# Kernel optimization log

Measured on AMD Instinct MI355X. Metric: run time of the kernel, lower is better.

The kernel has to match this reference:

```python
import jax, jax.numpy as jnp
import numpy as np

TEMP1, TEMP2, TEMP3 = 4.0, 5.0, 10.0  # forward() default temps
EPS = 1e-8


def setup_inputs() -> dict:
    key = jax.random.key(0)
    k1, k2 = jax.random.split(key)
    B, L, D = 64, 64, 512
    return {
        "ecg_embs": jax.random.normal(k1, (B, L, D), dtype=jnp.float32),
        "sent_embs": jax.random.normal(k2, (B, L, D), dtype=jnp.float32),
    }


def reference(ecg_embs, sent_embs):
    # Fully-batched version of the original per-sample Python loop.
    # i indexes the sentence (query) sample, j the ecg (context) sample.
    B, L, D = ecg_embs.shape
    # scores[i,j,s,q] = <ecg[j,s,:], sent[i,q,:]>  == contextT @ query in torch
    scores = jnp.einsum('jsd,iqd->ijsq', ecg_embs, sent_embs)
    # 1st softmax over query axis q
    attn = jax.nn.softmax(scores, axis=-1)
    # transpose to (i,j,q,s), temperature-scale, 2nd softmax over source axis s
    attn = jax.nn.softmax(TEMP1 * jnp.swapaxes(attn, -1, -2), axis=-1)  # (i,j,q,s)
    # weightedContext[i,j,q,:] = sum_s attn[i,j,q,s] * ecg[j,s,:]
    wctx = jnp.einsum('ijqs,jsd->ijqd', attn, ecg_embs)
    sent = sent_embs[:, None]  # (i,1,q,d) broadcast over j
    w12 = jnp.sum(sent * wctx, axis=-1)
    w1 = jnp.linalg.norm(sent, axis=-1)
    w2 = jnp.linalg.norm(wctx, axis=-1)
    cos = w12 / jnp.maximum(w1 * w2, EPS)  # (i,j,q)
    # row_sim.mul_(temp2).exp_().sum(dim=1).log() ; similarities[j,i] (cat along dim=1)
    sim = TEMP3 * jnp.log(jnp.sum(jnp.exp(TEMP2 * cos), axis=-1)).T  # (j,i)
    labels = jnp.arange(B)
    logp0 = jax.nn.log_softmax(sim, axis=-1)
    logp1 = jax.nn.log_softmax(sim.T, axis=-1)
    loss0 = -jnp.mean(logp0[labels, labels])
    loss1 = -jnp.mean(logp1[labels, labels])
    # att_maps: list of attn[i] from iteration i == diagonal (i==j) attention,
    # each shaped (1, queryL, ih=1, iw=sourceL); stacked -> (B, 1, L, 1, L)
    att_maps = attn[labels, labels][:, None, :, None, :]
    return (loss0 + loss1) / 2.0, att_maps
```

## Files before the change

### kernel.cpp

```cpp
#include <hip/hip_runtime.h>
#include <math.h>

typedef __attribute__((ext_vector_type(8))) short short8;
typedef __attribute__((ext_vector_type(4))) float f32x4;
typedef unsigned int uint;
typedef unsigned short ushort;

#define T1 4.0f
#define T2 5.0f
#define T3 10.0f
#define EPSF 1e-8f
#define SST 68

__device__ inline ushort f2bf(float x) {
    union { float f; uint u; } a; a.f = x;
    uint r = a.u + 0x7FFFu + ((a.u >> 16) & 1u);
    return (ushort)(r >> 16);
}
__device__ inline float bf2f(ushort h) {
    union { uint u; float f; } a; a.u = ((uint)h) << 16;
    return a.f;
}

#define GLDS(gsrc, ldst) \
    __builtin_amdgcn_global_load_lds( \
        (const __attribute__((address_space(1))) uint*)(gsrc), \
        (__attribute__((address_space(3))) uint*)(ldst), 16, 0, 0)

__global__ __launch_bounds__(256) void prep_kernel(
        const float* __restrict__ ecg, const float* __restrict__ sent,
        char* __restrict__ EH, char* __restrict__ EL,
        char* __restrict__ SH, char* __restrict__ SL, float* __restrict__ w1) {
    __shared__ float partial[256];
    const int bid = blockIdx.x;
    const int tensor = bid >> 6, idx = bid & 63;
    const float* src = (tensor ? sent : ecg) + (size_t)idx * 32768;
    char* dh = (tensor ? SH : EH) + (size_t)idx * 65536;
    char* dl = (tensor ? SL : EL) + (size_t)idx * 65536;
    const int tid = threadIdx.x;
    const int r = tid & 63;
    float s2 = 0.f;
    #pragma unroll
    for (int it = 0; it < 4; it++) {
        int kc = it * 4 + (tid >> 6);
        const float* p = src + r * 512 + kc * 32;
        char* oh = dh + kc * 4096 + r * 64;
        char* ol = dl + kc * 4096 + r * 64;
        #pragma unroll
        for (int c = 0; c < 4; c++) {
            float4 v0 = *(const float4*)(p + c * 8);
            float4 v1 = *(const float4*)(p + c * 8 + 4);
            float x[8] = {v0.x, v0.y, v0.z, v0.w, v1.x, v1.y, v1.z, v1.w};
            uint hw[4], lw[4];
            #pragma unroll
            for (int e = 0; e < 4; e++) {
                float a0 = x[2 * e], a1 = x[2 * e + 1];
                ushort h0 = f2bf(a0), h1 = f2bf(a1);
                hw[e] = (uint)h0 | ((uint)h1 << 16);
                ushort l0 = f2bf(a0 - bf2f(h0)), l1 = f2bf(a1 - bf2f(h1));
                lw[e] = (uint)l0 | ((uint)l1 << 16);
                s2 += a0 * a0 + a1 * a1;
            }
            int phys = (c + (r >> 1)) & 3;
            uint4 H; H.x = hw[0]; H.y = hw[1]; H.z = hw[2]; H.w = hw[3];
            *(uint4*)(oh + phys * 16) = H;
            uint4 L; L.x = lw[0]; L.y = lw[1]; L.z = lw[2]; L.w = lw[3];
            *(uint4*)(ol + phys * 16) = L;
        }
    }
    partial[tid] = s2;
    __syncthreads();
    if (tensor == 1 && tid < 64) {
        float t = partial[tid] + partial[tid + 64] + partial[tid + 128] + partial[tid + 192];
        w1[idx * 64 + tid] = sqrtf(t);
    }
}

__global__ __launch_bounds__(256) void gprep_kernel(
        const char* __restrict__ EH, const char* __restrict__ EL, char* __restrict__ Gp) {
    __shared__ __align__(16) char lds[8192];
    const int j = blockIdx.x;
    const int tid = threadIdx.x;
    const int wv = tid >> 6, lane = tid & 63;
    const int wq = wv >> 1, wn = wv & 1;
    const int quad = lane >> 4, ln = lane & 15;
    const char* srcH = EH + (size_t)j * 65536 + wv * 1024 + lane * 16;
    const char* srcL = EL + (size_t)j * 65536 + wv * 1024 + lane * 16;

    int ao[2], bo[2];
    #pragma unroll
    for (int mi = 0; mi < 2; mi++) {
        int R = 32 * wq + 16 * mi + ln;
        ao[mi] = R * 64 + ((quad + (R >> 1)) & 3) * 16;
    }
    #pragma unroll
    for (int ni = 0; ni < 2; ni++) {
        int R = 32 * wn + 16 * ni + ln;
        bo[ni] = R * 64 + ((quad + (R >> 1)) & 3) * 16;
    }

    f32x4 acc[2][2];
    #pragma unroll
    for (int a = 0; a < 2; a++)
        #pragma unroll
        for (int b = 0; b < 2; b++) acc[a][b] = (f32x4){0.f, 0.f, 0.f, 0.f};

    for (int kc = 0; kc < 16; kc++) {
        GLDS(srcH + (size_t)kc * 4096, lds + wv * 1024);
        GLDS(srcL + (size_t)kc * 4096, lds + 4096 + wv * 1024);
        __syncthreads();
        short8 ah[2], al[2], bh[2], bl[2];
        #pragma unroll
        for (int mi = 0; mi < 2; mi++) {
            ah[mi] = *(const short8*)(lds + ao[mi]);
            al[mi] = *(const short8*)(lds + 4096 + ao[mi]);
        }
        #pragma unroll
        for (int ni = 0; ni < 2; ni++) {
            bh[ni] = *(const short8*)(lds + bo[ni]);
            bl[ni] = *(const short8*)(lds + 4096 + bo[ni]);
        }
        #pragma unroll
        for (int mi = 0; mi < 2; mi++)
            #pragma unroll
            for (int ni = 0; ni < 2; ni++) {
                acc[mi][ni] = __builtin_amdgcn_mfma_f32_16x16x32_bf16(ah[mi], bh[ni], acc[mi][ni], 0, 0, 0);
                acc[mi][ni] = __builtin_amdgcn_mfma_f32_16x16x32_bf16(ah[mi], bl[ni], acc[mi][ni], 0, 0, 0);
                acc[mi][ni] = __builtin_amdgcn_mfma_f32_16x16x32_bf16(al[mi], bh[ni], acc[mi][ni], 0, 0, 0);
            }
        __syncthreads();
    }
    #pragma unroll
    for (int mi = 0; mi < 2; mi++)
        #pragma unroll
        for (int ni = 0; ni < 2; ni++)
            #pragma unroll
            for (int r = 0; r < 4; r++) {
                int t = 32 * wq + 16 * mi + quad * 4 + r;
                int u = 32 * wn + 16 * ni + ln;
                float g = acc[mi][ni][r];
                ushort h = f2bf(g);
                ushort l = f2bf(g - bf2f(h));
                char* base = Gp + (size_t)j * 16384 + t * 128 + (((u >> 3) + t) & 7) * 16 + (u & 7) * 2;
                *(ushort*)base = h;
                *(ushort*)(base + 8192) = l;
            }
}

__global__ __launch_bounds__(256, 4) void pair_kernel(
        const char* __restrict__ EH, const char* __restrict__ EL,
        const char* __restrict__ SH, const char* __restrict__ SL,
        const char* __restrict__ Gp, const float* __restrict__ w1g,
        float* __restrict__ simval, float* __restrict__ out) {

    __shared__ __align__(16) char lds[33792];
    __shared__ __align__(16) float mz[64];
    __shared__ float w12all[256], w2all[256];

    const int tid = threadIdx.x;
    const int bn = blockIdx.x;
    const int xcd = bn & 7, slot = bn >> 3;
    const int T = xcd * 8 + (slot >> 4);
    const int wp = slot & 15;
    const int bi = (T >> 3) * 4 + (wp >> 2);
    const int bj = (T & 7) * 4 + (wp & 3);
    const int i0 = bi * 2, j0 = bj * 2;

    const int wv = tid >> 6, lane = tid & 63;
    const int wq = wv >> 1, wn = wv & 1;
    const int quad = lane >> 4, ln = lane & 15;

    int aoff[4], boff[4];
    #pragma unroll
    for (int mi = 0; mi < 4; mi++) {
        int R = 64 * (mi >> 1) + 32 * wq + 16 * (mi & 1) + ln;
        aoff[mi] = R * 64 + ((quad + (R >> 1)) & 3) * 16;
    }
    #pragma unroll
    for (int ni = 0; ni < 4; ni++) {
        int R = 64 * (ni >> 1) + 32 * wn + 16 * (ni & 1) + ln;
        boff[ni] = 16384 + R * 64 + ((quad + (R >> 1)) & 3) * 16;
    }

    const char* gA; const char* gB; int ldoff;
    if (wv == 0)      { gA = EH + (size_t)j0 * 65536;       gB = EH + (size_t)(j0 + 1) * 65536; ldoff = 0; }
    else if (wv == 1) { gA = EL + (size_t)j0 * 65536;       gB = EL + (size_t)(j0 + 1) * 65536; ldoff = 8192; }
    else if (wv == 2) { gA = SH + (size_t)i0 * 65536;       gB = SH + (size_t)(i0 + 1) * 65536; ldoff = 16384; }
    else              { gA = SL + (size_t)i0 * 65536;       gB = SL + (size_t)(i0 + 1) * 65536; ldoff = 24576; }
    gA += lane * 16; gB += lane * 16;

    f32x4 acc[4][4];
    #pragma unroll
    for (int a = 0; a < 4; a++)
        #pragma unroll
        for (int b = 0; b < 4; b++) acc[a][b] = (f32x4){0.f, 0.f, 0.f, 0.f};

    for (int kc = 0; kc < 16; kc++) {
        #pragma unroll
        for (int n = 0; n < 4; n++) GLDS(gA + n * 1024, lds + ldoff + n * 1024);
        #pragma unroll
        for (int n = 0; n < 4; n++) GLDS(gB + n * 1024, lds + ldoff + 4096 + n * 1024);
        gA += 4096; gB += 4096;
        __syncthreads();
        short8 bh[4], bl[4];
        #pragma unroll
        for (int ni = 0; ni < 4; ni++) {
            bh[ni] = *(const short8*)(lds + boff[ni]);
            bl[ni] = *(const short8*)(lds + boff[ni] + 8192);
        }
        #pragma unroll
        for (int mi = 0; mi < 4; mi++) {
            short8 ah = *(const short8*)(lds + aoff[mi]);
            short8 al = *(const short8*)(lds + aoff[mi] + 8192);
            #pragma unroll
            for (int ni = 0; ni < 4; ni++) {
                acc[mi][ni] = __builtin_amdgcn_mfma_f32_16x16x32_bf16(ah, bh[ni], acc[mi][ni], 0, 0, 0);
                acc[mi][ni] = __builtin_amdgcn_mfma_f32_16x16x32_bf16(ah, bl[ni], acc[mi][ni], 0, 0, 0);
                acc[mi][ni] = __builtin_amdgcn_mfma_f32_16x16x32_bf16(al, bh[ni], acc[mi][ni], 0, 0, 0);
            }
        }
        __syncthreads();
    }

    float* SsT = (float*)lds;
    float* yT  = (float*)lds;
    char*  Pb  = lds + 17408;

    #pragma unroll
    for (int pr = 0; pr < 4; pr++) {
        const int a = pr >> 1, b = pr & 1;
        const int i = i0 + b, j = j0 + a;

        #pragma unroll
        for (int dm = 0; dm < 2; dm++)
            #pragma unroll
            for (int dn = 0; dn < 2; dn++) {
                int s0 = 32 * wq + 16 * dm + quad * 4;
                int q  = 32 * wn + 16 * dn + ln;
                *(f32x4*)(SsT + q * SST + s0) = acc[2 * a + dm][2 * b + dn];
            }
        __syncthreads();

        {
            const int s = tid >> 2, c = tid & 3;
            float vv[16]; float m = -1e30f;
            #pragma unroll
            for (int t = 0; t < 16; t++) { vv[t] = SsT[(16 * c + t) * SST + s]; m = fmaxf(m, vv[t]); }
            m = fmaxf(m, __shfl_xor(m, 1));
            m = fmaxf(m, __shfl_xor(m, 2));
            float sum = 0.f;
            #pragma unroll
            for (int t = 0; t < 16; t++) sum += __expf(vv[t] - m);
            sum += __shfl_xor(sum, 1);
            sum += __shfl_xor(sum, 2);
            if (c == 0) mz[s] = m + __logf(sum);
        }
        __syncthreads();

        {
            const int q = tid >> 2, c = tid & 3;
            float sc[16], at[16];
            #pragma unroll
            for (int r4 = 0; r4 < 4; r4++)
                *(f32x4*)(sc + 4 * r4) = *(const f32x4*)(SsT + q * SST + 16 * c + 4 * r4);
            float mzv[16];
            #pragma unroll
            for (int r4 = 0; r4 < 4; r4++)
                *(f32x4*)(mzv + 4 * r4) = *(const f32x4*)(mz + 16 * c + 4 * r4);
            float m2 = -1e30f;
            #pragma unroll
            for (int t = 0; t < 16; t++) {
                at[t] = __expf(sc[t] - mzv[t]);
                m2 = fmaxf(m2, T1 * at[t]);
            }
            m2 = fmaxf(m2, __shfl_xor(m2, 1));
            m2 = fmaxf(m2, __shfl_xor(m2, 2));
            float sum = 0.f;
            #pragma unroll
            for (int t = 0; t < 16; t++) { at[t] = __expf(T1 * at[t] - m2); sum += at[t]; }
            sum += __shfl_xor(sum, 1);
            sum += __shfl_xor(sum, 2);
            float inv = 1.f / sum;
            float p12 = 0.f;
            #pragma unroll
            for (int t = 0; t < 16; t++) { at[t] *= inv; p12 += at[t] * sc[t]; }
            p12 += __shfl_xor(p12, 1);
            p12 += __shfl_xor(p12, 2);
            if (c == 0) w12all[pr * 64 + q] = p12;

            if (i == j) {
                float* om = out + 1 + (size_t)i * 4096;
                #pragma unroll
                for (int t = 0; t < 16; t++) om[q * 64 + c * 16 + t] = at[t];
            }

            uint hw[8], lw[8];
            #pragma unroll
            for (int e = 0; e < 8; e++) {
                ushort h0 = f2bf(at[2 * e]), h1 = f2bf(at[2 * e + 1]);
                hw[e] = (uint)h0 | ((uint)h1 << 16);
                ushort l0 = f2bf(at[2 * e] - bf2f(h0)), l1 = f2bf(at[2 * e + 1] - bf2f(h1));
                lw[e] = (uint)l0 | ((uint)l1 << 16);
            }
            int p0 = (2 * c + q) & 7, p1 = (2 * c + 1 + q) & 7;
            uint4 W;
            W.x = hw[0]; W.y = hw[1]; W.z = hw[2]; W.w = hw[3];
            *(uint4*)(Pb + q * 128 + p0 * 16) = W;
            W.x = hw[4]; W.y = hw[5]; W.z = hw[6]; W.w = hw[7];
            *(uint4*)(Pb + q * 128 + p1 * 16) = W;
            W.x = lw[0]; W.y = lw[1]; W.z = lw[2]; W.w = lw[3];
            *(uint4*)(Pb + 8192 + q * 128 + p0 * 16) = W;
            W.x = lw[4]; W.y = lw[5]; W.z = lw[6]; W.w = lw[7];
            *(uint4*)(Pb + 8192 + q * 128 + p1 * 16) = W;
        }
        __syncthreads();

        {
            const char* gs = Gp + (size_t)j * 16384 + tid * 64;
            char* gd = lds + tid * 64;
            uint4 g0 = *(const uint4*)(gs);
            uint4 g1 = *(const uint4*)(gs + 16);
            uint4 g2 = *(const uint4*)(gs + 32);
            uint4 g3 = *(const uint4*)(gs + 48);
            *(uint4*)(gd)      = g0;
            *(uint4*)(gd + 16) = g1;
            *(uint4*)(gd + 32) = g2;
            *(uint4*)(gd + 48) = g3;
        }
        __syncthreads();

        f32x4 acc2[2][2];
        #pragma unroll
        for (int x = 0; x < 2; x++)
            #pragma unroll
            for (int y = 0; y < 2; y++) acc2[x][y] = (f32x4){0.f, 0.f, 0.f, 0.f};
        #pragma unroll
        for (int ch = 0; ch < 2; ch++) {
            short8 pah[2], pal[2], gbh[2], gbl[2];
            #pragma unroll
            for (int m2i = 0; m2i < 2; m2i++) {
                int q = 32 * wq + 16 * m2i + ln;
                int ph = ((ch * 4 + quad) + q) & 7;
                pah[m2i] = *(const short8*)(Pb + q * 128 + ph * 16);
                pal[m2i] = *(const short8*)(Pb + 8192 + q * 128 + ph * 16);
            }
            #pragma unroll
            for (int n2i = 0; n2i < 2; n2i++) {
                int u = 32 * wn + 16 * n2i + ln;
                int ph = ((ch * 4 + quad) + u) & 7;
                gbh[n2i] = *(const short8*)(lds + u * 128 + ph * 16);
                gbl[n2i] = *(const short8*)(lds + 8192 + u * 128 + ph * 16);
            }
            #pragma unroll
            for (int m2i = 0; m2i < 2; m2i++)
                #pragma unroll
                for (int n2i = 0; n2i < 2; n2i++) {
                    acc2[m2i][n2i] = __builtin_amdgcn_mfma_f32_16x16x32_bf16(pah[m2i], gbh[n2i], acc2[m2i][n2i], 0, 0, 0);
                    acc2[m2i][n2i] = __builtin_amdgcn_mfma_f32_16x16x32_bf16(pah[m2i], gbl[n2i], acc2[m2i][n2i], 0, 0, 0);
                    acc2[m2i][n2i] = __builtin_amdgcn_mfma_f32_16x16x32_bf16(pal[m2i], gbh[n2i], acc2[m2i][n2i], 0, 0, 0);
                }
        }
        __syncthreads();

        #pragma unroll
        for (int m2i = 0; m2i < 2; m2i++)
            #pragma unroll
            for (int n2i = 0; n2i < 2; n2i++) {
                int q0 = 32 * wq + 16 * m2i + quad * 4;
                int t  = 32 * wn + 16 * n2i + ln;
                *(f32x4*)(yT + t * SST + q0) = acc2[m2i][n2i];
            }
        __syncthreads();

        {
            const int q = tid >> 2, c = tid & 3;
            int p0 = (2 * c + q) & 7, p1 = (2 * c + 1 + q) & 7;
            uint4 H0 = *(const uint4*)(Pb + q * 128 + p0 * 16);
            uint4 H1 = *(const uint4*)(Pb + q * 128 + p1 * 16);
            uint4 L0 = *(const uint4*)(Pb + 8192 + q * 128 + p0 * 16);
            uint4 L1 = *(const uint4*)(Pb + 8192 + q * 128 + p1 * 16);
            uint hw[8] = {H0.x,H0.y,H0.z,H0.w, H1.x,H1.y,H1.z,H1.w};
            uint lw[8] = {L0.x,L0.y,L0.z,L0.w, L1.x,L1.y,L1.z,L1.w};
            float s = 0.f;
            #pragma unroll
            for (int e = 0; e < 8; e++) {
                float q0v = bf2f((ushort)(hw[e] & 0xFFFFu)) + bf2f((ushort)(lw[e] & 0xFFFFu));
                float q1v = bf2f((ushort)(hw[e] >> 16))     + bf2f((ushort)(lw[e] >> 16));
                s += q0v * yT[(16 * c + 2 * e) * SST + q];
                s += q1v * yT[(16 * c + 2 * e + 1) * SST + q];
            }
            s += __shfl_xor(s, 1);
            s += __shfl_xor(s, 2);
            if (c == 0) w2all[pr * 64 + q] = s;
        }
        __syncthreads();
    }

    {
        const int pr = wv;
        const int ii = i0 + (pr & 1), jj = j0 + (pr >> 1);
        float w2 = sqrtf(fmaxf(w2all[pr * 64 + lane], 0.f));
        float cosv = w12all[pr * 64 + lane] / fmaxf(w1g[ii * 64 + lane] * w2, EPSF);
        float e = __expf(T2 * cosv);
        #pragma unroll
        for (int off = 32; off; off >>= 1) e += __shfl_down(e, off);
        if (lane == 0) simval[ii * 64 + jj] = T3 * __logf(e);
    }
}

__global__ __launch_bounds__(256) void loss_kernel(const float* __restrict__ val,
                                                   float* __restrict__ out) {
    __shared__ float v[4096];
    const int tid = threadIdx.x;
    #pragma unroll
    for (int k = 0; k < 4; k++)
        ((float4*)v)[tid + k * 256] = ((const float4*)val)[tid + k * 256];
    __syncthreads();
    if (tid < 64) {
        int i = tid;
        float rmax = -1e30f, cmax = -1e30f;
        for (int jj = 0; jj < 64; jj++) {
            rmax = fmaxf(rmax, v[i * 64 + jj]);
            cmax = fmaxf(cmax, v[jj * 64 + i]);
        }
        float rs = 0.f, cs = 0.f;
        for (int jj = 0; jj < 64; jj++) {
            rs += __expf(v[i * 64 + jj] - rmax);
            cs += __expf(v[jj * 64 + i] - cmax);
        }
        float rlse = rmax + __logf(rs);
        float clse = cmax + __logf(cs);
        float part = 2.f * v[i * 64 + i] - rlse - clse;
        #pragma unroll
        for (int off = 32; off; off >>= 1) part += __shfl_down(part, off);
        if (i == 0) out[0] = -part / 128.f;
    }
}

extern "C" void kernel_launch(void* const* d_in, const int* in_sizes, int n_in,
                              void* d_out, int out_size, void* d_ws, size_t ws_size,
                              hipStream_t stream) {
    (void)in_sizes; (void)n_in; (void)out_size; (void)ws_size;
    const float* ecg  = (const float*)d_in[0];
    const float* sent = (const float*)d_in[1];
    float* out = (float*)d_out;

    char* ws = (char*)d_ws;
    float* w1v  = (float*)ws;
    float* simv = (float*)(ws + 16384);
    char* EH = ws + 32768;
    char* EL = EH + (size_t)64 * 65536;
    char* SH = EL + (size_t)64 * 65536;
    char* SL = SH + (size_t)64 * 65536;
    char* Gp = SL + (size_t)64 * 65536;

    prep_kernel <<<128, 256, 0, stream>>>(ecg, sent, EH, EL, SH, SL, w1v);
    gprep_kernel<<<64,  256, 0, stream>>>(EH, EL, Gp);
    pair_kernel <<<1024, 256, 0, stream>>>(EH, EL, SH, SL, Gp, w1v, simv, out);
    loss_kernel <<<1,   256, 0, stream>>>(simv, out);
}
```

Before: 152.3 us.

## Switch pair kernel to 32x32 MFMA tiles and fold G prep into prep kernel

Both matrix products in the pair kernel now use 32x32x16 bf16 MFMA with 16-wide accumulators instead of 16x16x32 tiles, and the LDS fragment offsets are rewritten to match. The aim is fewer LDS fragment reads and MFMA issues per output. The separate gprep kernel is merged into the ecg half of prep_kernel, which saves a launch. That fused path now reads EH/EL straight from global memory that the same block has just written, and its correctness depends on global writes being visible within the block after the barrier. Two smaller changes: the Gp tile loads are issued early, before the softmax, to hide their latency, and the softmax column reads are staggered per thread group to reduce LDS bank conflicts.

Measured after the change: 156.7 us. +2.9%, slower.

```diff
diff --git a/kernel.cpp b/kernel.cpp
--- a/kernel.cpp
+++ b/kernel.cpp
@@ -3,6 +3,7 @@
 
 typedef __attribute__((ext_vector_type(8))) short short8;
 typedef __attribute__((ext_vector_type(4))) float f32x4;
+typedef __attribute__((ext_vector_type(16))) float f32x16;
 typedef unsigned int uint;
 typedef unsigned short ushort;
 
@@ -30,7 +31,8 @@
 __global__ __launch_bounds__(256) void prep_kernel(
         const float* __restrict__ ecg, const float* __restrict__ sent,
         char* __restrict__ EH, char* __restrict__ EL,
-        char* __restrict__ SH, char* __restrict__ SL, float* __restrict__ w1) {
+        char* __restrict__ SH, char* __restrict__ SL,
+        char* __restrict__ Gp, float* __restrict__ w1) {
     __shared__ float partial[256];
     const int bid = blockIdx.x;
     const int tensor = bid >> 6, idx = bid & 63;
@@ -70,81 +72,79 @@
     }
     partial[tid] = s2;
     __syncthreads();
-    if (tensor == 1 && tid < 64) {
-        float t = partial[tid] + partial[tid + 64] + partial[tid + 128] + partial[tid + 192];
-        w1[idx * 64 + tid] = sqrtf(t);
-    }
-}
-
-__global__ __launch_bounds__(256) void gprep_kernel(
-        const char* __restrict__ EH, const char* __restrict__ EL, char* __restrict__ Gp) {
-    __shared__ __align__(16) char lds[8192];
-    const int j = blockIdx.x;
-    const int tid = threadIdx.x;
-    const int wv = tid >> 6, lane = tid & 63;
-    const int wq = wv >> 1, wn = wv & 1;
-    const int quad = lane >> 4, ln = lane & 15;
-    const char* srcH = EH + (size_t)j * 65536 + wv * 1024 + lane * 16;
-    const char* srcL = EL + (size_t)j * 65536 + wv * 1024 + lane * 16;
-
-    int ao[2], bo[2];
-    #pragma unroll
-    for (int mi = 0; mi < 2; mi++) {
-        int R = 32 * wq + 16 * mi + ln;
-        ao[mi] = R * 64 + ((quad + (R >> 1)) & 3) * 16;
-    }
-    #pragma unroll
-    for (int ni = 0; ni < 2; ni++) {
-        int R = 32 * wn + 16 * ni + ln;
-        bo[ni] = R * 64 + ((quad + (R >> 1)) & 3) * 16;
-    }
-
-    f32x4 acc[2][2];
-    #pragma unroll
-    for (int a = 0; a < 2; a++)
-        #pragma unroll
-        for (int b = 0; b < 2; b++) acc[a][b] = (f32x4){0.f, 0.f, 0.f, 0.f};
-
-    for (int kc = 0; kc < 16; kc++) {
-        GLDS(srcH + (size_t)kc * 4096, lds + wv * 1024);
-        GLDS(srcL + (size_t)kc * 4096, lds + 4096 + wv * 1024);
-        __syncthreads();
-        short8 ah[2], al[2], bh[2], bl[2];
+    if (tensor == 1) {
+        if (tid < 64) {
+            float t = partial[tid] + partial[tid + 64] + partial[tid + 128] + partial[tid + 192];
+            w1[idx * 64 + tid] = sqrtf(t);
+        }
+        return;
+    }
+
+    {
+        const char* srcH = EH + (size_t)idx * 65536;
+        const char* srcL = EL + (size_t)idx * 65536;
+        const int wv = tid >> 6, lane = tid & 63;
+        const int wq = wv >> 1, wn = wv & 1;
+        const int quad = lane >> 4, ln = lane & 15;
+
+        int ao[2], bo[2];
         #pragma unroll
         for (int mi = 0; mi < 2; mi++) {
-            ah[mi] = *(const short8*)(lds + ao[mi]);
-            al[mi] = *(const short8*)(lds + 4096 + ao[mi]);
+            int R = 32 * wq + 16 * mi + ln;
+            ao[mi] = R * 64 + ((quad + (R >> 1)) & 3) * 16;
         }
         #pragma unroll
         for (int ni = 0; ni < 2; ni++) {
-            bh[ni] = *(const short8*)(lds + bo[ni]);
-            bl[ni] = *(const short8*)(lds + 4096 + bo[ni]);
+            int R = 32 * wn + 16 * ni + ln;
+            bo[ni] = R * 64 + ((quad + (R >> 1)) & 3) * 16;
+        }
+
+        f32x4 acc[2][2];
+        #pragma unroll
+        for (int a = 0; a < 2; a++)
+            #pragma unroll
+            for (int b = 0; b < 2; b++) acc[a][b] = (f32x4){0.f, 0.f, 0.f, 0.f};
+
+        #pragma unroll 2
+        for (int kc = 0; kc < 16; kc++) {
+            const char* ph = srcH + (size_t)kc * 4096;
+            const char* pl = srcL + (size_t)kc * 4096;
+            short8 ah[2], al[2], bh[2], bl[2];
+            #pragma unroll
+            for (int mi = 0; mi < 2; mi++) {
+                ah[mi] = *(const short8*)(ph + ao[mi]);
+                al[mi] = *(const short8*)(pl + ao[mi]);
+            }
+            #pragma unroll
+            for (int ni = 0; ni < 2; ni++) {
+                bh[ni] = *(const short8*)(ph + bo[ni]);
+                bl[ni] = *(const short8*)(pl + bo[ni]);
+            }
+            #pragma unroll
+            for (int mi = 0; mi < 2; mi++)
+                #pragma unroll
+                for (int ni = 0; ni < 2; ni++) {
+                    acc[mi][ni] = __builtin_amdgcn_mfma_f32_16x16x32_bf16(ah[mi], bh[ni], acc[mi][ni], 0, 0, 0);
+                    acc[mi][ni] = __builtin_amdgcn_mfma_f32_16x16x32_bf16(ah[mi], bl[ni], acc[mi][ni], 0, 0, 0);
+                    acc[mi][ni] = __builtin_amdgcn_mfma_f32_16x16x32_bf16(al[mi], bh[ni], acc[mi][ni], 0, 0, 0);
+                }
         }
         #pragma unroll
         for (int mi = 0; mi < 2; mi++)
             #pragma unroll
-            for (int ni = 0; ni < 2; ni++) {
-                acc[mi][ni] = __builtin_amdgcn_mfma_f32_16x16x32_bf16(ah[mi], bh[ni], acc[mi][ni], 0, 0, 0);
-                acc[mi][ni] = __builtin_amdgcn_mfma_f32_16x16x32_bf16(ah[mi], bl[ni], acc[mi][ni], 0, 0, 0);
-                acc[mi][ni] = __builtin_amdgcn_mfma_f32_16x16x32_bf16(al[mi], bh[ni], acc[mi][ni], 0, 0, 0);
-            }
-        __syncthreads();
-    }
-    #pragma unroll
-    for (int mi = 0; mi < 2; mi++)
-        #pragma unroll
-        for (int ni = 0; ni < 2; ni++)
-            #pragma unroll
-            for (int r = 0; r < 4; r++) {
-                int t = 32 * wq + 16 * mi + quad * 4 + r;
-                int u = 32 * wn + 16 * ni + ln;
-                float g = acc[mi][ni][r];
-                ushort h = f2bf(g);
-                ushort l = f2bf(g - bf2f(h));
-                char* base = Gp + (size_t)j * 16384 + t * 128 + (((u >> 3) + t) & 7) * 16 + (u & 7) * 2;
-                *(ushort*)base = h;
-                *(ushort*)(base + 8192) = l;
-            }
+            for (int ni = 0; ni < 2; ni++)
+                #pragma unroll
+                for (int rr = 0; rr < 4; rr++) {
+                    int t = 32 * wq + 16 * mi + quad * 4 + rr;
+                    int u = 32 * wn + 16 * ni + ln;
+                    float g = acc[mi][ni][rr];
+                    ushort h = f2bf(g);
+                    ushort l = f2bf(g - bf2f(h));
+                    char* base = Gp + (size_t)idx * 16384 + t * 128 + (((u >> 3) + t) & 7) * 16 + (u & 7) * 2;
+                    *(ushort*)base = h;
+                    *(ushort*)(base + 8192) = l;
+                }
+    }
 }
 
 __global__ __launch_bounds__(256, 4) void pair_kernel(
@@ -168,19 +168,19 @@
 
     const int wv = tid >> 6, lane = tid & 63;
     const int wq = wv >> 1, wn = wv & 1;
-    const int quad = lane >> 4, ln = lane & 15;
-
-    int aoff[4], boff[4];
+    const int l5 = lane >> 5, l31 = lane & 31;
+
+    int aoff[2][2], boff[2][2];
     #pragma unroll
-    for (int mi = 0; mi < 4; mi++) {
-        int R = 64 * (mi >> 1) + 32 * wq + 16 * (mi & 1) + ln;
-        aoff[mi] = R * 64 + ((quad + (R >> 1)) & 3) * 16;
-    }
-    #pragma unroll
-    for (int ni = 0; ni < 4; ni++) {
-        int R = 64 * (ni >> 1) + 32 * wn + 16 * (ni & 1) + ln;
-        boff[ni] = 16384 + R * 64 + ((quad + (R >> 1)) & 3) * 16;
-    }
+    for (int ti = 0; ti < 2; ti++)
+        #pragma unroll
+        for (int kh = 0; kh < 2; kh++) {
+            int cc = l5 + 2 * kh;
+            int Ra = 64 * ti + 32 * wq + l31;
+            aoff[ti][kh] = Ra * 64 + ((cc + (Ra >> 1)) & 3) * 16;
+            int Rb = 64 * ti + 32 * wn + l31;
+            boff[ti][kh] = 16384 + Rb * 64 + ((cc + (Rb >> 1)) & 3) * 16;
+        }
 
     const char* gA; const char* gB; int ldoff;
     if (wv == 0)      { gA = EH + (size_t)j0 * 65536;       gB = EH + (size_t)(j0 + 1) * 65536; ldoff = 0; }
@@ -189,11 +189,9 @@
     else              { gA = SL + (size_t)i0 * 65536;       gB = SL + (size_t)(i0 + 1) * 65536; ldoff = 24576; }
     gA += lane * 16; gB += lane * 16;
 
-    f32x4 acc[4][4];
-    #pragma unroll
-    for (int a = 0; a < 4; a++)
-        #pragma unroll
-        for (int b = 0; b < 4; b++) acc[a][b] = (f32x4){0.f, 0.f, 0.f, 0.f};
+    const f32x16 zf = {0.f,0.f,0.f,0.f,0.f,0.f,0.f,0.f,0.f,0.f,0.f,0.f,0.f,0.f,0.f,0.f};
+    f32x16 acc[2][2];
+    acc[0][0] = zf; acc[0][1] = zf; acc[1][0] = zf; acc[1][1] = zf;
 
     for (int kc = 0; kc < 16; kc++) {
         #pragma unroll
@@ -202,22 +200,30 @@
         for (int n = 0; n < 4; n++) GLDS(gB + n * 1024, lds + ldoff + 4096 + n * 1024);
         gA += 4096; gB += 4096;
         __syncthreads();
-        short8 bh[4], bl[4];
-        #pragma unroll
-        for (int ni = 0; ni < 4; ni++) {
-            bh[ni] = *(const short8*)(lds + boff[ni]);
-            bl[ni] = *(const short8*)(lds + boff[ni] + 8192);
-        }
-        #pragma unroll
-        for (int mi = 0; mi < 4; mi++) {
-            short8 ah = *(const short8*)(lds + aoff[mi]);
-            short8 al = *(const short8*)(lds + aoff[mi] + 8192);
-            #pragma unroll
-            for (int ni = 0; ni < 4; ni++) {
-                acc[mi][ni] = __builtin_amdgcn_mfma_f32_16x16x32_bf16(ah, bh[ni], acc[mi][ni], 0, 0, 0);
-                acc[mi][ni] = __builtin_amdgcn_mfma_f32_16x16x32_bf16(ah, bl[ni], acc[mi][ni], 0, 0, 0);
-                acc[mi][ni] = __builtin_amdgcn_mfma_f32_16x16x32_bf16(al, bh[ni], acc[mi][ni], 0, 0, 0);
-            }
+        short8 bh[2][2], bl[2][2];
+        #pragma unroll
+        for (int ni = 0; ni < 2; ni++)
+            #pragma unroll
+            for (int kh = 0; kh < 2; kh++) {
+                bh[ni][kh] = *(const short8*)(lds + boff[ni][kh]);
+                bl[ni][kh] = *(const short8*)(lds + boff[ni][kh] + 8192);
+            }
+        #pragma unroll
+        for (int mi = 0; mi < 2; mi++) {
+            short8 ah[2], al[2];
+            #pragma unroll
+            for (int kh = 0; kh < 2; kh++) {
+                ah[kh] = *(const short8*)(lds + aoff[mi][kh]);
+                al[kh] = *(const short8*)(lds + aoff[mi][kh] + 8192);
+            }
+            #pragma unroll
+            for (int ni = 0; ni < 2; ni++)
+                #pragma unroll
+                for (int kh = 0; kh < 2; kh++) {
+                    acc[mi][ni] = __builtin_amdgcn_mfma_f32_32x32x16_bf16(ah[kh], bh[ni][kh], acc[mi][ni], 0, 0, 0);
+                    acc[mi][ni] = __builtin_amdgcn_mfma_f32_32x32x16_bf16(ah[kh], bl[ni][kh], acc[mi][ni], 0, 0, 0);
+                    acc[mi][ni] = __builtin_amdgcn_mfma_f32_32x32x16_bf16(al[kh], bh[ni][kh], acc[mi][ni], 0, 0, 0);
+                }
         }
         __syncthreads();
     }
@@ -231,21 +237,33 @@
         const int a = pr >> 1, b = pr & 1;
         const int i = i0 + b, j = j0 + a;
 
-        #pragma unroll
-        for (int dm = 0; dm < 2; dm++)
-            #pragma unroll
-            for (int dn = 0; dn < 2; dn++) {
-                int s0 = 32 * wq + 16 * dm + quad * 4;
-                int q  = 32 * wn + 16 * dn + ln;
-                *(f32x4*)(SsT + q * SST + s0) = acc[2 * a + dm][2 * b + dn];
-            }
+        const char* gs = Gp + (size_t)j * 16384 + tid * 16;
+        uint4 g0 = *(const uint4*)(gs);
+        uint4 g1 = *(const uint4*)(gs + 4096);
+        uint4 g2 = *(const uint4*)(gs + 8192);
+        uint4 g3 = *(const uint4*)(gs + 12288);
+
+        {
+            f32x16 v = acc[a][b];
+            int q = 32 * wn + l31;
+            #pragma unroll
+            for (int g = 0; g < 4; g++) {
+                int s0 = 32 * wq + 4 * l5 + 8 * g;
+                *(f32x4*)(SsT + q * SST + s0) =
+                    (f32x4){v[4 * g], v[4 * g + 1], v[4 * g + 2], v[4 * g + 3]};
+            }
+        }
         __syncthreads();
 
         {
             const int s = tid >> 2, c = tid & 3;
             float vv[16]; float m = -1e30f;
             #pragma unroll
-            for (int t = 0; t < 16; t++) { vv[t] = SsT[(16 * c + t) * SST + s]; m = fmaxf(m, vv[t]); }
+            for (int t = 0; t < 16; t++) {
+                int tt = (t + 4 * c) & 15;
+                vv[t] = SsT[(16 * c + tt) * SST + s];
+                m = fmaxf(m, vv[t]);
+            }
             m = fmaxf(m, __shfl_xor(m, 1));
             m = fmaxf(m, __shfl_xor(m, 2));
             float sum = 0.f;
@@ -316,60 +334,41 @@
         __syncthreads();
 
         {
-            const char* gs = Gp + (size_t)j * 16384 + tid * 64;
-            char* gd = lds + tid * 64;
-            uint4 g0 = *(const uint4*)(gs);
-            uint4 g1 = *(const uint4*)(gs + 16);
-            uint4 g2 = *(const uint4*)(gs + 32);
-            uint4 g3 = *(const uint4*)(gs + 48);
-            *(uint4*)(gd)      = g0;
-            *(uint4*)(gd + 16) = g1;
-            *(uint4*)(gd + 32) = g2;
-            *(uint4*)(gd + 48) = g3;
-        }
-        __syncthreads();
-
-        f32x4 acc2[2][2];
-        #pragma unroll
-        for (int x = 0; x < 2; x++)
-            #pragma unroll
-            for (int y = 0; y < 2; y++) acc2[x][y] = (f32x4){0.f, 0.f, 0.f, 0.f};
-        #pragma unroll
-        for (int ch = 0; ch < 2; ch++) {
-            short8 pah[2], pal[2], gbh[2], gbl[2];
-            #pragma unroll
-            for (int m2i = 0; m2i < 2; m2i++) {
-                int q = 32 * wq + 16 * m2i + ln;
-                int ph = ((ch * 4 + quad) + q) & 7;
-                pah[m2i] = *(const short8*)(Pb + q * 128 + ph * 16);
-                pal[m2i] = *(const short8*)(Pb + 8192 + q * 128 + ph * 16);
-            }
-            #pragma unroll
-            for (int n2i = 0; n2i < 2; n2i++) {
-                int u = 32 * wn + 16 * n2i + ln;
-                int ph = ((ch * 4 + quad) + u) & 7;
-                gbh[n2i] = *(const short8*)(lds + u * 128 + ph * 16);
-                gbl[n2i] = *(const short8*)(lds + 8192 + u * 128 + ph * 16);
-            }
-            #pragma unroll
-            for (int m2i = 0; m2i < 2; m2i++)
-                #pragma unroll
-                for (int n2i = 0; n2i < 2; n2i++) {
-                    acc2[m2i][n2i] = __builtin_amdgcn_mfma_f32_16x16x32_bf16(pah[m2i], gbh[n2i], acc2[m2i][n2i], 0, 0, 0);
-                    acc2[m2i][n2i] = __builtin_amdgcn_mfma_f32_16x16x32_bf16(pah[m2i], gbl[n2i], acc2[m2i][n2i], 0, 0, 0);
-                    acc2[m2i][n2i] = __builtin_amdgcn_mfma_f32_16x16x32_bf16(pal[m2i], gbh[n2i], acc2[m2i][n2i], 0, 0, 0);
-                }
-        }
-        __syncthreads();
-
-        #pragma unroll
-        for (int m2i = 0; m2i < 2; m2i++)
-            #pragma unroll
-            for (int n2i = 0; n2i < 2; n2i++) {
-                int q0 = 32 * wq + 16 * m2i + quad * 4;
-                int t  = 32 * wn + 16 * n2i + ln;
-                *(f32x4*)(yT + t * SST + q0) = acc2[m2i][n2i];
-            }
+            char* gd = lds + tid * 16;
+            *(uint4*)(gd)          = g0;
+            *(uint4*)(gd + 4096)   = g1;
+            *(uint4*)(gd + 8192)   = g2;
+            *(uint4*)(gd + 12288)  = g3;
+        }
+        __syncthreads();
+
+        f32x16 acc2 = zf;
+        #pragma unroll
+        for (int ks = 0; ks < 4; ks++) {
+            int cc = l5 + 2 * ks;
+            int q = 32 * wq + l31;
+            int php = (cc + q) & 7;
+            short8 pah = *(const short8*)(Pb + q * 128 + php * 16);
+            short8 pal = *(const short8*)(Pb + 8192 + q * 128 + php * 16);
+            int u = 32 * wn + l31;
+            int phg = (cc + u) & 7;
+            short8 gbh = *(const short8*)(lds + u * 128 + phg * 16);
+            short8 gbl = *(const short8*)(lds + 8192 + u * 128 + phg * 16);
+            acc2 = __builtin_amdgcn_mfma_f32_32x32x16_bf16(pah, gbh, acc2, 0, 0, 0);
+            acc2 = __builtin_amdgcn_mfma_f32_32x32x16_bf16(pah, gbl, acc2, 0, 0, 0);
+            acc2 = __builtin_amdgcn_mfma_f32_32x32x16_bf16(pal, gbh, acc2, 0, 0, 0);
+        }
+        __syncthreads();
+
+        {
+            int t = 32 * wn + l31;
+            #pragma unroll
+            for (int g = 0; g < 4; g++) {
+                int q0 = 32 * wq + 4 * l5 + 8 * g;
+                *(f32x4*)(yT + t * SST + q0) =
+                    (f32x4){acc2[4 * g], acc2[4 * g + 1], acc2[4 * g + 2], acc2[4 * g + 3]};
+            }
+        }
         __syncthreads();
 
         {
@@ -454,8 +453,7 @@
     char* SL = SH + (size_t)64 * 65536;
     char* Gp = SL + (size_t)64 * 65536;
 
-    prep_kernel <<<128, 256, 0, stream>>>(ecg, sent, EH, EL, SH, SL, w1v);
-    gprep_kernel<<<64,  256, 0, stream>>>(EH, EL, Gp);
+    prep_kernel <<<128, 256, 0, stream>>>(ecg, sent, EH, EL, SH, SL, Gp, w1v);
     pair_kernel <<<1024, 256, 0, stream>>>(EH, EL, SH, SL, Gp, w1v, simv, out);
     loss_kernel <<<1,   256, 0, stream>>>(simv, out);
 }
```
